# Optimization experiments

Hardware: AMD Instinct MI355X
Metric: run time of the kernel (lower is better)

## Reference

```python
import jax, jax.numpy as jnp
import numpy as np

B = 16384            # batch
F = 26               # number of categorical fields (columns of x)
FIELD_DIM = 100000   # vocab per field
D = 64               # base_embedding_dim
BLOCK_FIELDS = [list(range(0, 8)), list(range(8, 16)), list(range(16, 26))]
BLOCK_DIMS = [64, 32, 16]   # block 0 == base dim -> identity projector


def setup_inputs() -> dict:
    key = jax.random.key(0)
    ks = jax.random.split(key, 8)
    x = jax.random.randint(ks[0], (B, F), 0, FIELD_DIM, dtype=jnp.int32)
    # per-block embedding tables: rows = sum of field_dims of the block's fields
    t0 = jax.random.normal(ks[1], (len(BLOCK_FIELDS[0]) * FIELD_DIM, BLOCK_DIMS[0]), jnp.float32) * 0.02
    t1 = jax.random.normal(ks[2], (len(BLOCK_FIELDS[1]) * FIELD_DIM, BLOCK_DIMS[1]), jnp.float32) * 0.02
    t2 = jax.random.normal(ks[3], (len(BLOCK_FIELDS[2]) * FIELD_DIM, BLOCK_DIMS[2]), jnp.float32) * 0.02
    # projectors for blocks whose dim != base dim (torch Linear: y = x @ W.T + b)
    W1 = jax.random.normal(ks[4], (D, BLOCK_DIMS[1]), jnp.float32) * 0.05
    b1 = jnp.zeros((D,), jnp.float32)
    W2 = jax.random.normal(ks[5], (D, BLOCK_DIMS[2]), jnp.float32) * 0.05
    b2 = jnp.zeros((D,), jnp.float32)
    return {"x": x, "t0": t0, "t1": t1, "t2": t2, "W1": W1, "b1": b1, "W2": W2, "b2": b2}


def reference(x, t0, t1, t2, W1, b1, W2, b2):
    tables = [t0, t1, t2]
    projs = [None, (W1, b1), (W2, b2)]
    out = jnp.zeros((x.shape[0], D), dtype=t0.dtype)
    for blk in range(len(BLOCK_FIELDS)):
        fields = np.asarray(BLOCK_FIELDS[blk])                 # static column routing
        offs = jnp.arange(len(fields), dtype=x.dtype) * FIELD_DIM  # per-field row offsets
        idx = x[:, fields] + offs[None, :]                     # [B, nb]
        emb = tables[blk][idx]                                 # gather -> [B, nb, d_blk]
        if projs[blk] is not None:
            W, b = projs[blk]
            emb = jnp.einsum('bnd,od->bno', emb, W) + b        # project to base dim
        out = out + emb.sum(axis=1)                            # segment-sum over block's fields
    return out
```

## Files before the change

### kernel.cpp

```cpp
#include <hip/hip_runtime.h>
#include <hip/hip_bf16.h>

#define BATCH 16384
#define NFIELDS 26
#define FIELD_DIM 100000


__device__ __forceinline__ float ntload(const float* p) {
    return __builtin_nontemporal_load(p);
}

__global__ __launch_bounds__(256, 6) void mixdim_embbag_kernel(
    const int* __restrict__ x,
    const float* __restrict__ t0,
    const float* __restrict__ t1,
    const float* __restrict__ t2,
    const float* __restrict__ W1,
    const float* __restrict__ b1,
    const float* __restrict__ W2,
    const float* __restrict__ b2,
    float* __restrict__ out)
{
    __shared__ float ldsW[48 * 64];

    const int tid  = threadIdx.x;
    const int lane = tid & 63;
    const int wave = tid >> 6;
    const int row0 = (blockIdx.x * 4 + wave) * 2;

    #pragma unroll
    for (int i = 0; i < 8; ++i) {
        const int e = tid * 8 + i;
        ldsW[(e & 31) * 64 + (e >> 5)] = W1[e];
    }
    #pragma unroll
    for (int i = 0; i < 4; ++i) {
        const int e = tid * 4 + i;
        ldsW[2048 + (e & 15) * 64 + (e >> 4)] = W2[e];
    }

    int xi = 0;
    {
        const int l = lane & 31;
        const int r = lane >> 5;
        if (l < NFIELDS) xi = x[(row0 + r) * NFIELDS + l];
    }

    __syncthreads();

    float acc0 = 0.f, acc1 = 0.f;

    #pragma unroll
    for (int f = 0; f < 8; ++f) {
        const int i0 = __shfl(xi, f)      + f * FIELD_DIM;
        const int i1 = __shfl(xi, 32 + f) + f * FIELD_DIM;
        acc0 += ntload(t0 + i0 * 64 + lane);
        acc1 += ntload(t0 + i1 * 64 + lane);
    }

    float s1_0 = 0.f, s1_1 = 0.f;
    {
        const int d1 = lane & 31;
        #pragma unroll
        for (int j = 0; j < 8; ++j) {
            const int i0 = __shfl(xi, 8 + j)      + j * FIELD_DIM;
            const int i1 = __shfl(xi, 32 + 8 + j) + j * FIELD_DIM;
            s1_0 += ntload(t1 + i0 * 32 + d1);
            s1_1 += ntload(t1 + i1 * 32 + d1);
        }
    }

    float s2_0 = 0.f, s2_1 = 0.f;
    {
        const int d2 = lane & 15;
        #pragma unroll
        for (int j = 0; j < 10; ++j) {
            const int i0 = __shfl(xi, 16 + j)      + j * FIELD_DIM;
            const int i1 = __shfl(xi, 32 + 16 + j) + j * FIELD_DIM;
            s2_0 += ntload(t2 + i0 * 16 + d2);
            s2_1 += ntload(t2 + i1 * 16 + d2);
        }
    }

    #pragma unroll
    for (int k = 0; k < 32; ++k) {
        const float w = ldsW[k * 64 + lane];
        acc0 += __shfl(s1_0, k) * w;
        acc1 += __shfl(s1_1, k) * w;
    }
    #pragma unroll
    for (int k = 0; k < 16; ++k) {
        const float w = ldsW[2048 + k * 64 + lane];
        acc0 += __shfl(s2_0, k) * w;
        acc1 += __shfl(s2_1, k) * w;
    }

    const float bias = 8.0f * b1[lane] + 10.0f * b2[lane];
    out[row0 * 64 + lane]       = acc0 + bias;
    out[(row0 + 1) * 64 + lane] = acc1 + bias;
}

extern "C" void kernel_launch(void* const* d_in, const int* in_sizes, int n_in,
                              void* d_out, int out_size, void* d_ws, size_t ws_size,
                              hipStream_t stream) {
    const int*   x  = (const int*)  d_in[0];
    const float* t0 = (const float*)d_in[1];
    const float* t1 = (const float*)d_in[2];
    const float* t2 = (const float*)d_in[3];
    const float* W1 = (const float*)d_in[4];
    const float* b1 = (const float*)d_in[5];
    const float* W2 = (const float*)d_in[6];
    const float* b2 = (const float*)d_in[7];
    float* out = (float*)d_out;

    dim3 grid(BATCH / 8);
    dim3 block(256);
    hipLaunchKernelGGL(mixdim_embbag_kernel, grid, block, 0, stream,
                       x, t0, t1, t2, W1, b1, W2, b2, out);
}
```

Measured before the change: 321.2 us.

## Vectorize embedding gathers to 16-byte loads with four rows per wave

Result: no change. 316.4 us, median of 2 (-1.5%).

```diff
diff --git a/kernel.cpp b/kernel.cpp
--- a/kernel.cpp
+++ b/kernel.cpp
@@ -1,16 +1,17 @@
 #include <hip/hip_runtime.h>
-#include <hip/hip_bf16.h>
 
 #define BATCH 16384
 #define NFIELDS 26
 #define FIELD_DIM 100000
 
 
-__device__ __forceinline__ float ntload(const float* p) {
-    return __builtin_nontemporal_load(p);
+typedef float f32x4 __attribute__((ext_vector_type(4)));
+
+__device__ __forceinline__ f32x4 ntload4(const float* p) {
+    return __builtin_nontemporal_load((const f32x4*)p);
 }
 
-__global__ __launch_bounds__(256, 6) void mixdim_embbag_kernel(
+__global__ __launch_bounds__(256, 4) void mixdim_embbag_kernel(
     const int* __restrict__ x,
     const float* __restrict__ t0,
     const float* __restrict__ t1,
@@ -21,83 +22,96 @@
     const float* __restrict__ b2,
     float* __restrict__ out)
 {
-    __shared__ float ldsW[48 * 64];
+    __shared__ float ldsW1[32 * 64];
+    __shared__ float ldsW2[16 * 64];
+    __shared__ int   ldsX[16 * NFIELDS];
 
     const int tid  = threadIdx.x;
     const int lane = tid & 63;
     const int wave = tid >> 6;
-    const int row0 = (blockIdx.x * 4 + wave) * 2;
 
     #pragma unroll
     for (int i = 0; i < 8; ++i) {
         const int e = tid * 8 + i;
-        ldsW[(e & 31) * 64 + (e >> 5)] = W1[e];
+        ldsW1[(e & 31) * 64 + (e >> 5)] = W1[e];
     }
     #pragma unroll
     for (int i = 0; i < 4; ++i) {
         const int e = tid * 4 + i;
-        ldsW[2048 + (e & 15) * 64 + (e >> 4)] = W2[e];
+        ldsW2[(e & 15) * 64 + (e >> 4)] = W2[e];
     }
-
-    int xi = 0;
-    {
-        const int l = lane & 31;
-        const int r = lane >> 5;
-        if (l < NFIELDS) xi = x[(row0 + r) * NFIELDS + l];
-    }
+    ldsX[tid] = x[blockIdx.x * (16 * NFIELDS) + tid];
+    if (tid < 16 * NFIELDS - 256)
+        ldsX[tid + 256] = x[blockIdx.x * (16 * NFIELDS) + tid + 256];
 
     __syncthreads();
 
-    float acc0 = 0.f, acc1 = 0.f;
+    const int g = lane >> 4;
+    const int q = lane & 15;
+    const int xbase = wave * 4 * NFIELDS;
+    const int rowbase = blockIdx.x * 16 + wave * 4;
+
+    f32x4 acc = {0.f, 0.f, 0.f, 0.f};
 
     #pragma unroll
     for (int f = 0; f < 8; ++f) {
-        const int i0 = __shfl(xi, f)      + f * FIELD_DIM;
-        const int i1 = __shfl(xi, 32 + f) + f * FIELD_DIM;
-        acc0 += ntload(t0 + i0 * 64 + lane);
-        acc1 += ntload(t0 + i1 * 64 + lane);
+        const int idx = ldsX[xbase + g * NFIELDS + f] + f * FIELD_DIM;
+        acc += ntload4(t0 + idx * 64 + q * 4);
     }
 
-    float s1_0 = 0.f, s1_1 = 0.f;
+    float s1a[4] = {0.f, 0.f, 0.f, 0.f};
     {
-        const int d1 = lane & 31;
+        const int h  = lane >> 5;
+        const int r1 = (lane >> 3) & 3;
+        const int c1 = lane & 7;
         #pragma unroll
-        for (int j = 0; j < 8; ++j) {
-            const int i0 = __shfl(xi, 8 + j)      + j * FIELD_DIM;
-            const int i1 = __shfl(xi, 32 + 8 + j) + j * FIELD_DIM;
-            s1_0 += ntload(t1 + i0 * 32 + d1);
-            s1_1 += ntload(t1 + i1 * 32 + d1);
+        for (int jj = 0; jj < 4; ++jj) {
+            const int f = 8 + jj * 2 + h;
+            const int idx = ldsX[xbase + r1 * NFIELDS + f] + (f - 8) * FIELD_DIM;
+            const f32x4 v = ntload4(t1 + idx * 32 + c1 * 4);
+            s1a[0] += v.x; s1a[1] += v.y; s1a[2] += v.z; s1a[3] += v.w;
         }
     }
 
-    float s2_0 = 0.f, s2_1 = 0.f;
+    float s2a[4] = {0.f, 0.f, 0.f, 0.f};
     {
-        const int d2 = lane & 15;
+        const int qd = lane >> 4;
+        const int r2 = (lane >> 2) & 3;
+        const int c2 = lane & 3;
         #pragma unroll
-        for (int j = 0; j < 10; ++j) {
-            const int i0 = __shfl(xi, 16 + j)      + j * FIELD_DIM;
-            const int i1 = __shfl(xi, 32 + 16 + j) + j * FIELD_DIM;
-            s2_0 += ntload(t2 + i0 * 16 + d2);
-            s2_1 += ntload(t2 + i1 * 16 + d2);
+        for (int jj = 0; jj < 3; ++jj) {
+            const int f = 16 + jj * 4 + qd;
+            if (f < 26) {
+                const int idx = ldsX[xbase + r2 * NFIELDS + f] + (f - 16) * FIELD_DIM;
+                const f32x4 v = ntload4(t2 + idx * 16 + c2 * 4);
+                s2a[0] += v.x; s2a[1] += v.y; s2a[2] += v.z; s2a[3] += v.w;
+            }
         }
     }
 
     #pragma unroll
+    for (int c = 0; c < 4; ++c) {
+        s1a[c] += __shfl_xor(s1a[c], 32);
+        s2a[c] += __shfl_xor(s2a[c], 16);
+        s2a[c] += __shfl_xor(s2a[c], 32);
+    }
+
+    const f32x4* W1v = (const f32x4*)ldsW1;
+    const f32x4* W2v = (const f32x4*)ldsW2;
+    #pragma unroll
     for (int k = 0; k < 32; ++k) {
-        const float w = ldsW[k * 64 + lane];
-        acc0 += __shfl(s1_0, k) * w;
-        acc1 += __shfl(s1_1, k) * w;
+        const float v = __shfl(s1a[k & 3], g * 8 + (k >> 2));
+        acc += W1v[k * 16 + q] * v;
     }
     #pragma unroll
     for (int k = 0; k < 16; ++k) {
-        const float w = ldsW[2048 + k * 64 + lane];
-        acc0 += __shfl(s2_0, k) * w;
-        acc1 += __shfl(s2_1, k) * w;
+        const float v = __shfl(s2a[k & 3], g * 4 + (k >> 2));
+        acc += W2v[k * 16 + q] * v;
     }
 
-    const float bias = 8.0f * b1[lane] + 10.0f * b2[lane];
-    out[row0 * 64 + lane]       = acc0 + bias;
-    out[(row0 + 1) * 64 + lane] = acc1 + bias;
+    const f32x4 bias = ((const f32x4*)b1)[q] * 8.0f + ((const f32x4*)b2)[q] * 10.0f;
+    const int row = rowbase + g;
+    *(f32x4*)(out + row * 64 + q * 4) = acc + bias;
 }
 
 extern "C" void kernel_launch(void* const* d_in, const int* in_sizes, int n_in,
@@ -113,7 +127,7 @@
     const float* b2 = (const float*)d_in[7];
     float* out = (float*)d_out;
 
-    dim3 grid(BATCH / 8);
+    dim3 grid(BATCH / 16);
     dim3 block(256);
     hipLaunchKernelGGL(mixdim_embbag_kernel, grid, block, 0, stream,
                        x, t0, t1, t2, W1, b1, W2, b2, out);
```
